# Performance work log

Measured on AMD Instinct MI355X. Metric: run time of the kernel, lower is better.

The kernel has to match this reference:

```python
import jax, jax.numpy as jnp
import numpy as np

NUM_HEADS = 16
HEAD_DIM = 128
WINDOW = 512
ROPE_BASE = 10000.0


def _rope_cos_sin(seq_len):
    inv_freq = 1.0 / (ROPE_BASE ** (jnp.arange(0, HEAD_DIM, 2, dtype=jnp.float32) / HEAD_DIM))
    freqs = jnp.arange(seq_len, dtype=jnp.float32)[:, None] * inv_freq[None, :]  # (s, d/2)
    return jnp.cos(freqs), jnp.sin(freqs)


def _apply_rotary(x, cos, sin):
    # x: (b, h, s, d); cos/sin: (s, d/2). Interleaved pairs as in the torch impl.
    x1, x2 = x[..., ::2], x[..., 1::2]
    c = cos[None, None]
    s = sin[None, None]
    r1 = x1 * c - x2 * s
    r2 = x1 * s + x2 * c
    return jnp.stack([r1, r2], axis=-1).reshape(x.shape)


def setup_inputs() -> dict:
    key = jax.random.key(0)
    ks = jax.random.split(key, 5)
    dim = NUM_HEADS * HEAD_DIM
    x = jax.random.normal(ks[0], (1, 4096, dim), dtype=jnp.float32)
    std = 0.02
    Wq = jax.random.normal(ks[1], (dim, dim), dtype=jnp.float32) * std
    Wk = jax.random.normal(ks[2], (dim, dim), dtype=jnp.float32) * std
    Wv = jax.random.normal(ks[3], (dim, dim), dtype=jnp.float32) * std
    Wo = jax.random.normal(ks[4], (dim, dim), dtype=jnp.float32) * std
    return {"x": x, "Wq": Wq, "Wk": Wk, "Wv": Wv, "Wo": Wo}


def reference(x, Wq, Wk, Wv, Wo):
    b, s, dim = x.shape
    scale = HEAD_DIM ** -0.5

    def split_heads(t):
        return t.reshape(b, s, NUM_HEADS, HEAD_DIM).transpose(0, 2, 1, 3)  # b h s d

    q = split_heads(x @ Wq.T)
    k = split_heads(x @ Wk.T)
    v = split_heads(x @ Wv.T)

    cos, sin = _rope_cos_sin(s)
    q = _apply_rotary(q, cos, sin)
    k = _apply_rotary(k, cos, sin)

    scores = jnp.einsum('bhqd,bhkd->bhqk', q, k) * scale  # (b, h, s, s)
    pos = jnp.arange(s)
    i, j = pos[:, None], pos[None, :]
    mask = (j <= i) & (i - j < WINDOW)  # sliding-window causal
    scores = jnp.where(mask[None, None], scores, -jnp.inf)
    attn = jax.nn.softmax(scores, axis=-1)

    out = jnp.einsum('bhqk,bhkd->bhqd', attn, v)
    out = out.transpose(0, 2, 1, 3).reshape(b, s, dim)
    return out @ Wo.T
```

## Files before the change

kernel.cpp:

```cpp
#include <hip/hip_runtime.h>
#include <hip/hip_bf16.h>
#include <math.h>

#define DIM 2048
#define NH 16
#define HD 128
#define WIN 512

typedef __hip_bfloat16 bf16;
using frag8 = __attribute__((ext_vector_type(8))) short;
using facc4 = __attribute__((ext_vector_type(4))) float;

__device__ inline float toF(const bf16 v) { return __bfloat162float(v); }
template <typename T> __device__ inline T fromF(float v);
template <> __device__ inline float fromF<float>(float v) { return v; }
template <> __device__ inline bf16 fromF<bf16>(float v) { return __float2bfloat16(v); }

__device__ inline unsigned bfb(float x) {
    unsigned u = __float_as_uint(x);
    u += 0x7fffu + ((u >> 16) & 1u);
    return u >> 16;
}

__device__ inline uint4 pack8(const float* p) {
    const float4 v0 = *(const float4*)p;
    const float4 v1 = *(const float4*)(p + 4);
    uint4 r;
    r.x = bfb(v0.x) | (bfb(v0.y) << 16);
    r.y = bfb(v0.z) | (bfb(v0.w) << 16);
    r.z = bfb(v1.x) | (bfb(v1.y) << 16);
    r.w = bfb(v1.z) | (bfb(v1.w) << 16);
    return r;
}

__global__ __launch_bounds__(256) void cvt_f32_bf16(const float* __restrict__ src,
                                                    bf16* __restrict__ dst, int n8) {
    const int i = blockIdx.x * 256 + threadIdx.x;
    if (i < n8) ((uint4*)dst)[i] = pack8(src + (size_t)i * 8);
}

#define W8LOG 19
__global__ __launch_bounds__(256) void cvt4_f32_bf16(const float* __restrict__ s0,
                                                     const float* __restrict__ s1,
                                                     const float* __restrict__ s2,
                                                     const float* __restrict__ s3,
                                                     bf16* __restrict__ dst) {
    const int i = blockIdx.x * 256 + threadIdx.x;
    const int seg = i >> W8LOG;
    const int off = i & ((1 << W8LOG) - 1);
    const float* s = (seg == 0) ? s0 : (seg == 1) ? s1 : (seg == 2) ? s2 : s3;
    ((uint4*)dst)[i] = pack8(s + (size_t)off * 8);
}

__device__ inline void gload_lds16(const bf16* g, short* l) {
    __builtin_amdgcn_global_load_lds(
        (const __attribute__((address_space(1))) unsigned int*)g,
        (__attribute__((address_space(3))) unsigned int*)l, 16, 0, 0);
}


#define WAIT_LGKM0()                                             \
    do {                                                         \
        asm volatile("s_waitcnt lgkmcnt(0)" ::: "memory");       \
        __builtin_amdgcn_sched_barrier(0);                       \
    } while (0)

#define READ_A(BUF, MI)                                                          \
    do {                                                                         \
        _Pragma("unroll") for (int ii = 0; ii < 4; ++ii)                         \
        _Pragma("unroll") for (int kk = 0; kk < 2; ++kk) {                       \
            const int row_ = wm * 128 + (MI) * 64 + ii * 16 + mr;                \
            const int slot_ = ((kk << 2) + q) ^ (row_ & 7);                      \
            a[ii][kk] = *(const frag8*)&lds[BUF][0][row_][slot_ << 3];           \
        }                                                                        \
    } while (0)

#define READ_B(BUF, NI)                                                          \
    do {                                                                         \
        _Pragma("unroll") for (int jj = 0; jj < 2; ++jj)                         \
        _Pragma("unroll") for (int kk = 0; kk < 2; ++kk) {                       \
            const int row_ = wn * 64 + (NI) * 32 + jj * 16 + mr;                 \
            const int slot_ = ((kk << 2) + q) ^ (row_ & 7);                      \
            b[NI][jj][kk] = *(const frag8*)&lds[BUF][1][row_][slot_ << 3];       \
        }                                                                        \
    } while (0)

#define MFMA_QUAD(MI, NI)                                                        \
    do {                                                                         \
        __builtin_amdgcn_s_setprio(1);                                           \
        _Pragma("unroll") for (int ii = 0; ii < 4; ++ii)                         \
        _Pragma("unroll") for (int jj = 0; jj < 2; ++jj)                         \
        _Pragma("unroll") for (int kk = 0; kk < 2; ++kk)                         \
            acc[(MI) * 4 + ii][(NI) * 2 + jj] =                                  \
                __builtin_amdgcn_mfma_f32_16x16x32_bf16(                         \
                    a[ii][kk], b[NI][jj][kk], acc[(MI) * 4 + ii][(NI) * 2 + jj], \
                    0, 0, 0);                                                    \
        __builtin_amdgcn_s_setprio(0);                                           \
    } while (0)

template <typename TC, bool SPLIT>
__global__ __launch_bounds__(512, 2) void gemm256_8ph(const bf16* __restrict__ A,
                                                      const bf16* __restrict__ B,
                                                      TC* __restrict__ C,
                                                      bf16* __restrict__ Qp,
                                                      bf16* __restrict__ Kp,
                                                      bf16* __restrict__ Vp,
                                                      int M, int N, int K) {
    __shared__ __align__(16) short lds[2][2][256][64];
    const int tid = threadIdx.x;
    const int lane = tid & 63;
    const int w = tid >> 6;

    const int gx = gridDim.x;
    const int nwg = gx * (int)gridDim.y;
    const int lin0 = (int)blockIdx.y * gx + (int)blockIdx.x;
    const int lin = ((nwg & 7) == 0) ? (lin0 & 7) * (nwg >> 3) + (lin0 >> 3) : lin0;
    const int n0 = (lin % gx) * 256;
    const int m0 = (lin / gx) * 256;

    const int wm = w >> 2, wn = w & 3;
    const int q = lane >> 4, mr = lane & 15;
    const int sl = lane & 7, rlo = lane >> 3;
    const int rbA = wm * 128 + wn * 16;
    const int rbB = (w >> 1) * 64 + (w & 1) * 16;

    const int nt = K >> 6;
    const int nIter = nt >> 1;

    facc4 acc[8][4];
#pragma unroll
    for (int i = 0; i < 8; ++i)
#pragma unroll
        for (int j = 0; j < 4; ++j)
#pragma unroll
            for (int r = 0; r < 4; ++r) acc[i][j][r] = 0.f;

    frag8 a[4][2], b[2][2][2];

    auto stage = [&](const bf16* __restrict__ G, int grb, int mat, int buf, int ub, int t) {
        const int kt = t < nt ? t : nt - 1;
        const int k0 = kt << 6;
#pragma unroll
        for (int u = 0; u < 2; ++u) {
            const int row0 = ub + u * 8;
            const int row = row0 + rlo;
            gload_lds16(G + (size_t)(grb + row) * K + k0 + ((sl ^ rlo) << 3),
                        (short*)&lds[buf][mat][row0][0]);
        }
    };

    stage(A, m0, 0, 0, rbA, 0);
    stage(A, m0, 0, 0, rbA + 64, 0);
    stage(B, n0, 1, 0, rbB, 0);
    stage(B, n0, 1, 0, rbB + 32, 0);
    stage(A, m0, 0, 1, rbA, 1);
    stage(B, n0, 1, 1, rbB, 1);
    stage(B, n0, 1, 1, rbB + 32, 1);
    asm volatile("s_waitcnt vmcnt(6)" ::: "memory");
    __builtin_amdgcn_s_barrier();

    for (int it = 0; it < nIter; ++it) {
        const int t2 = 2 * it + 2;
        READ_A(0, 0);
        READ_B(0, 0);
        stage(A, m0, 0, 1, rbA + 64, 2 * it + 1);
        __builtin_amdgcn_s_barrier();
        WAIT_LGKM0();
        MFMA_QUAD(0, 0);
        __builtin_amdgcn_s_barrier();
        READ_B(0, 1);
        stage(A, m0, 0, 0, rbA, t2);
        __builtin_amdgcn_s_barrier();
        WAIT_LGKM0();
        MFMA_QUAD(0, 1);
        __builtin_amdgcn_s_barrier();
        READ_A(0, 1);
        stage(B, n0, 1, 0, rbB, t2);
        __builtin_amdgcn_s_barrier();
        WAIT_LGKM0();
        MFMA_QUAD(1, 0);
        __builtin_amdgcn_s_barrier();
        stage(B, n0, 1, 0, rbB + 32, t2);
        __builtin_amdgcn_s_barrier();
        __builtin_amdgcn_sched_barrier(0);
        MFMA_QUAD(1, 1);
        asm volatile("s_waitcnt vmcnt(6)" ::: "memory");
        __builtin_amdgcn_s_barrier();
        READ_A(1, 0);
        READ_B(1, 0);
        stage(A, m0, 0, 0, rbA + 64, t2);
        __builtin_amdgcn_s_barrier();
        WAIT_LGKM0();
        MFMA_QUAD(0, 0);
        __builtin_amdgcn_s_barrier();
        READ_B(1, 1);
        stage(A, m0, 0, 1, rbA, t2 + 1);
        __builtin_amdgcn_s_barrier();
        WAIT_LGKM0();
        MFMA_QUAD(0, 1);
        __builtin_amdgcn_s_barrier();
        READ_A(1, 1);
        stage(B, n0, 1, 1, rbB, t2 + 1);
        __builtin_amdgcn_s_barrier();
        WAIT_LGKM0();
        MFMA_QUAD(1, 0);
        __builtin_amdgcn_s_barrier();
        stage(B, n0, 1, 1, rbB + 32, t2 + 1);
        __builtin_amdgcn_s_barrier();
        __builtin_amdgcn_sched_barrier(0);
        MFMA_QUAD(1, 1);
        asm volatile("s_waitcnt vmcnt(6)" ::: "memory");
        __builtin_amdgcn_s_barrier();
    }

    if (SPLIT) {
        if (n0 < 2 * DIM) {
            bf16* dst = (n0 < DIM) ? Qp : Kp;
            const int nb = n0 % DIM;
            const int row0 = m0 + wm * 128 + q * 4;
#pragma unroll
            for (int jn = 0; jn < 4; ++jn) {
                const int col = nb + wn * 64 + jn * 16 + mr;
                const int f = (col & 127) >> 1;
                const float inv = __expf(-0.14391157f * (float)f);
                const float sgn = (col & 1) ? 1.f : -1.f;
                float cb_, sb_, c1, s1, c16, s16;
                sincosf((float)row0 * inv, &sb_, &cb_);
                sincosf(inv, &s1, &c1);
                sincosf(16.f * inv, &s16, &c16);
#pragma unroll
                for (int im = 0; im < 8; ++im) {
                    float c = cb_, s = sb_;
#pragma unroll
                    for (int r = 0; r < 4; ++r) {
                        const float v = acc[im][jn][r];
                        const float p = __shfl_xor(v, 1, 64);
                        dst[(size_t)(row0 + im * 16 + r) * DIM + col] =
                            fromF<bf16>(v * c + sgn * p * s);
                        const float cn = c * c1 - s * s1;
                        const float sn = s * c1 + c * s1;
                        c = cn; s = sn;
                    }
                    const float cbn = cb_ * c16 - sb_ * s16;
                    const float sbn = sb_ * c16 + cb_ * s16;
                    cb_ = cbn; sb_ = sbn;
                }
            }
        } else {
            asm volatile("s_waitcnt vmcnt(0)" ::: "memory");
            __builtin_amdgcn_s_barrier();
            short* sc = (short*)lds;
            const int cb = n0 - 2 * DIM;
            const int colR = tid >> 2;
#pragma unroll
            for (int half = 0; half < 2; ++half) {
                if (half) __builtin_amdgcn_s_barrier();
                if ((wn >> 1) == half) {
#pragma unroll
                    for (int im = 0; im < 8; ++im) {
                        const int s = wm * 128 + im * 16 + q * 4;
#pragma unroll
                        for (int jn = 0; jn < 4; ++jn) {
                            const int cl = (wn & 1) * 64 + jn * 16 + mr;
                            uint2 pk;
                            pk.x = bfb(acc[im][jn][0]) | (bfb(acc[im][jn][1]) << 16);
                            pk.y = bfb(acc[im][jn][2]) | (bfb(acc[im][jn][3]) << 16);
                            *(uint2*)&sc[cl * 264 + s] = pk;
                        }
                    }
                }
                __builtin_amdgcn_s_barrier();
#pragma unroll
                for (int rr = 0; rr < 8; ++rr) {
                    const int s0 = (tid & 3) * 8 + rr * 32;
                    const uint4 v = *(const uint4*)&sc[colR * 264 + s0];
                    *(uint4*)(Vp + (size_t)(cb + half * 128 + colR) * M + m0 + s0) = v;
                }
            }
        }
    } else {
#pragma unroll
        for (int im = 0; im < 8; ++im)
#pragma unroll
            for (int jn = 0; jn < 4; ++jn) {
                const int col = n0 + wn * 64 + jn * 16 + mr;
#pragma unroll
                for (int r = 0; r < 4; ++r) {
                    const int row = m0 + wm * 128 + im * 16 + q * 4 + r;
                    C[(size_t)row * N + col] = fromF<TC>(acc[im][jn][r]);
                }
            }
    }
}

template <typename TC>
__global__ __launch_bounds__(256) void gemm_bt_async(const bf16* __restrict__ A,
                                                     const bf16* __restrict__ B,
                                                     TC* __restrict__ C,
                                                     int M, int N, int K) {
    __shared__ short As[128 * 32];
    __shared__ short Bs[128 * 32];
    const int tid = threadIdx.x;
    const int lane = tid & 63;
    const int w = tid >> 6;
    const int m0 = blockIdx.y * 128;
    const int n0 = blockIdx.x * 128;
    const int wm = (w >> 1) * 64;
    const int wn = (w & 1) * 64;
    const int q = lane >> 4;
    const int mr = lane & 15;

    facc4 acc[4][4];
#pragma unroll
    for (int i = 0; i < 4; ++i)
#pragma unroll
        for (int j = 0; j < 4; ++j)
#pragma unroll
            for (int r = 0; r < 4; ++r) acc[i][j][r] = 0.f;

    for (int k0 = 0; k0 < K; k0 += 32) {
        __syncthreads();
#pragma unroll
        for (int u = 0; u < 2; ++u) {
            const int c = w * 128 + u * 64 + lane;
            const int row = c >> 2, col = (c & 3) * 8;
            gload_lds16(A + (size_t)(m0 + row) * K + k0 + col, As + (w * 128 + u * 64) * 8);
            gload_lds16(B + (size_t)(n0 + row) * K + k0 + col, Bs + (w * 128 + u * 64) * 8);
        }
        __syncthreads();

        frag8 af[4], bfr[4];
#pragma unroll
        for (int i = 0; i < 4; ++i)
            af[i] = *(const frag8*)&As[(wm + 16 * i + mr) * 32 + q * 8];
#pragma unroll
        for (int j = 0; j < 4; ++j)
            bfr[j] = *(const frag8*)&Bs[(wn + 16 * j + mr) * 32 + q * 8];
#pragma unroll
        for (int i = 0; i < 4; ++i)
#pragma unroll
            for (int j = 0; j < 4; ++j)
                acc[i][j] = __builtin_amdgcn_mfma_f32_16x16x32_bf16(af[i], bfr[j], acc[i][j], 0, 0, 0);
    }

#pragma unroll
    for (int i = 0; i < 4; ++i)
#pragma unroll
        for (int j = 0; j < 4; ++j) {
            const int col = n0 + wn + 16 * j + mr;
#pragma unroll
            for (int r = 0; r < 4; ++r) {
                const int row = m0 + wm + 16 * i + q * 4 + r;
                C[(size_t)row * N + col] = fromF<TC>(acc[i][j][r]);
            }
        }
}

__global__ __launch_bounds__(256, 2) void flash_swa(const bf16* __restrict__ Q,
                                                    const bf16* __restrict__ K,
                                                    const bf16* __restrict__ Vt,
                                                    bf16* __restrict__ O, int S) {
    __shared__ __align__(16) char lds[74752];
    short* Ksl = (short*)lds;
    short* Vtl = (short*)(lds + 32768);
    short* Ps  = (short*)(lds + 65536);

    const int tid = threadIdx.x;
    const int lane = tid & 63;
    const int w = tid >> 6;
    const int q = lane >> 4;
    const int mr = lane & 15;
    const int bx = blockIdx.x;
    const int i0 = (((bx & 7) << 3) | (bx >> 3)) * 64;
    const int h = blockIdx.y;
    const float scale = 0.08838834764831845f;
    const int sw = mr & 7;

    frag8 qf[4];
    const bf16* qptr = Q + (size_t)(i0 + w * 16 + mr) * DIM + h * HD + q * 8;
#pragma unroll
    for (int kk = 0; kk < 4; ++kk) qf[kk] = *(const frag8*)(qptr + kk * 32);

    const bf16* vtg = Vt + (size_t)h * HD * S;

    int koff[4], voff[4];
#pragma unroll
    for (int u = 0; u < 4; ++u) {
        const int krow = w * 16 + 4 * u + (lane >> 4);
        const int kch = (lane & 15) ^ (krow & 7);
        koff[u] = krow * DIM + h * HD + kch * 8;
        const int vrow = w * 32 + 8 * u + (lane >> 3);
        const int vch = (lane & 7) ^ (vrow & 7);
        voff[u] = vrow * S + vch * 8;
    }

    auto issue = [&](int t, int buf) {
        int jb = i0 - WIN + t * 64;
        if (jb > S - 64) jb = S - 64;
        const bf16* kb = K + (size_t)jb * DIM;
        const bf16* vb = vtg + jb;
#pragma unroll
        for (int u = 0; u < 4; ++u)
            gload_lds16(kb + koff[u], Ksl + buf * 8192 + (w * 16 + 4 * u) * 128);
#pragma unroll
        for (int u = 0; u < 4; ++u)
            gload_lds16(vb + voff[u], Vtl + buf * 8192 + (w * 32 + 8 * u) * 64);
    };

    float mrow[4], lrow[4];
    facc4 oacc[8];
#pragma unroll
    for (int r = 0; r < 4; ++r) { mrow[r] = -1e30f; lrow[r] = 0.f; }
#pragma unroll
    for (int dt = 0; dt < 8; ++dt)
#pragma unroll
        for (int r = 0; r < 4; ++r) oacc[dt][r] = 0.f;

    const int t0 = (i0 >= WIN) ? 0 : (WIN - i0) / 64;
    issue(t0, 0);
    issue(t0 + 1, 1);
    int p = 0;

    for (int t = t0; t < 9; ++t) {
        const int jb = i0 - WIN + t * 64;
        asm volatile("s_waitcnt vmcnt(8)" ::: "memory");
        __builtin_amdgcn_s_barrier();
        __builtin_amdgcn_sched_barrier(0);

        facc4 sacc[4];
#pragma unroll
        for (int nt = 0; nt < 4; ++nt)
#pragma unroll
            for (int r = 0; r < 4; ++r) sacc[nt][r] = 0.f;
        __builtin_amdgcn_s_setprio(1);
#pragma unroll
        for (int nt = 0; nt < 4; ++nt) {
#pragma unroll
            for (int kk = 0; kk < 4; ++kk) {
                const frag8 kfr = *(const frag8*)&Ksl[p * 8192 + (nt * 16 + mr) * 128 +
                                                      (((kk * 4 + q) ^ sw) << 3)];
                sacc[nt] = __builtin_amdgcn_mfma_f32_16x16x32_bf16(qf[kk], kfr, sacc[nt], 0, 0, 0);
            }
        }
        __builtin_amdgcn_s_setprio(0);

        float sv[4][4];
        float rmax[4] = {-1e30f, -1e30f, -1e30f, -1e30f};
#pragma unroll
        for (int nt = 0; nt < 4; ++nt) {
            const int j = jb + nt * 16 + mr;
#pragma unroll
            for (int r = 0; r < 4; ++r) {
                const int i = i0 + w * 16 + q * 4 + r;
                const bool valid = (j <= i) && (i - j < WIN);
                sv[nt][r] = valid ? sacc[nt][r] * scale : -1e30f;
                rmax[r] = fmaxf(rmax[r], sv[nt][r]);
            }
        }
#pragma unroll
        for (int msk = 1; msk <= 8; msk <<= 1)
#pragma unroll
            for (int r = 0; r < 4; ++r)
                rmax[r] = fmaxf(rmax[r], __shfl_xor(rmax[r], msk, 64));

        float alpha[4], rsum[4];
#pragma unroll
        for (int r = 0; r < 4; ++r) {
            const float mn = fmaxf(mrow[r], rmax[r]);
            alpha[r] = __expf(mrow[r] - mn);
            mrow[r] = mn;
            rsum[r] = 0.f;
        }
#pragma unroll
        for (int nt = 0; nt < 4; ++nt)
#pragma unroll
            for (int r = 0; r < 4; ++r) {
                const float pv = (sv[nt][r] > -1e29f) ? __expf(sv[nt][r] - mrow[r]) : 0.f;
                rsum[r] += pv;
                Ps[(w * 16 + q * 4 + r) * 72 + nt * 16 + mr] = (short)bfb(pv);
            }
#pragma unroll
        for (int msk = 1; msk <= 8; msk <<= 1)
#pragma unroll
            for (int r = 0; r < 4; ++r)
                rsum[r] += __shfl_xor(rsum[r], msk, 64);
#pragma unroll
        for (int r = 0; r < 4; ++r) lrow[r] = lrow[r] * alpha[r] + rsum[r];
#pragma unroll
        for (int dt = 0; dt < 8; ++dt)
#pragma unroll
            for (int r = 0; r < 4; ++r) oacc[dt][r] *= alpha[r];

        __builtin_amdgcn_s_setprio(1);
#pragma unroll
        for (int ks = 0; ks < 2; ++ks) {
            const frag8 pf = *(const frag8*)&Ps[(w * 16 + mr) * 72 + ks * 32 + q * 8];
#pragma unroll
            for (int dt = 0; dt < 8; ++dt) {
                const frag8 vf = *(const frag8*)&Vtl[p * 8192 + (dt * 16 + mr) * 64 +
                                                     (((ks * 4 + q) ^ sw) << 3)];
                oacc[dt] = __builtin_amdgcn_mfma_f32_16x16x32_bf16(pf, vf, oacc[dt], 0, 0, 0);
            }
        }
        __builtin_amdgcn_s_setprio(0);

        __builtin_amdgcn_s_barrier();
        __builtin_amdgcn_sched_barrier(0);
        issue(t + 2, p);
        p ^= 1;
    }
    asm volatile("s_waitcnt vmcnt(0)" ::: "memory");

    float inv[4];
#pragma unroll
    for (int r = 0; r < 4; ++r) inv[r] = 1.0f / lrow[r];
#pragma unroll
    for (int dt = 0; dt < 8; ++dt)
#pragma unroll
        for (int r = 0; r < 4; ++r) {
            const int row = i0 + w * 16 + q * 4 + r;
            O[(size_t)row * DIM + h * HD + dt * 16 + mr] = fromF<bf16>(oacc[dt][r] * inv[r]);
        }
}

extern "C" void kernel_launch(void* const* d_in, const int* in_sizes, int n_in,
                              void* d_out, int out_size, void* d_ws, size_t ws_size,
                              hipStream_t stream) {
    const float* x  = (const float*)d_in[0];
    const float* Wq = (const float*)d_in[1];
    const float* Wk = (const float*)d_in[2];
    const float* Wv = (const float*)d_in[3];
    const float* Wo = (const float*)d_in[4];
    float* out = (float*)d_out;

    const int S = in_sizes[0] / DIM;
    const size_t elems = (size_t)S * DIM;
    const size_t wsz = (size_t)DIM * DIM;

    bf16* Q    = (bf16*)d_ws;
    bf16* K    = Q + elems;
    bf16* V    = K + elems;
    bf16* Aat  = V + elems;
    bf16* xb   = Aat + elems;
    bf16* Wcat = xb + elems;
    bf16* Wob  = Wcat + 3 * wsz;

    cvt_f32_bf16<<<(int)(elems / 8 / 256), 256, 0, stream>>>(x, xb, (int)(elems / 8));
    cvt4_f32_bf16<<<(int)(4 * wsz / 8 / 256), 256, 0, stream>>>(Wq, Wk, Wv, Wo, Wcat);

    gemm256_8ph<bf16, true><<<dim3(3 * DIM / 256, S / 256), 512, 0, stream>>>(
        xb, Wcat, (bf16*)nullptr, Q, K, V, S, 3 * DIM, DIM);

    flash_swa<<<dim3(S / 64, NH), 256, 0, stream>>>(Q, K, V, Aat, S);

    gemm_bt_async<float><<<dim3(DIM / 128, S / 128), 256, 0, stream>>>(
        Aat, Wob, out, S, DIM, DIM);
}
```

Before: 375.5 us.

## Enlarge flash SWA query tile to 256 rows with 8 waves, two row groups each

Each flash-attention block now handles 256 query rows with 8 waves, and each wave processes two 16-row groups. This lets each K/V tile loaded into LDS be reused across four times as many queries, and the V fragment is shared across both groups in the PV MFMA loop. The block-to-(head, query tile) mapping is also reworked so neighbouring blocks share K/V from adjacent heads. In exchange, the key-tile loop runs 12 iterations instead of 9 to cover the wider window, so more partially masked tiles are computed. Register pressure and LDS use per block also rise, which may reduce occupancy.

```diff
diff --git a/kernel.cpp b/kernel.cpp
--- a/kernel.cpp
+++ b/kernel.cpp
@@ -356,11 +356,11 @@
         }
 }
 
-__global__ __launch_bounds__(256, 2) void flash_swa(const bf16* __restrict__ Q,
+__global__ __launch_bounds__(512, 2) void flash_swa(const bf16* __restrict__ Q,
                                                     const bf16* __restrict__ K,
                                                     const bf16* __restrict__ Vt,
                                                     bf16* __restrict__ O, int S) {
-    __shared__ __align__(16) char lds[74752];
+    __shared__ __align__(16) char lds[102400];
     short* Ksl = (short*)lds;
     short* Vtl = (short*)(lds + 32768);
     short* Ps  = (short*)(lds + 65536);
@@ -370,28 +370,29 @@
     const int w = tid >> 6;
     const int q = lane >> 4;
     const int mr = lane & 15;
-    const int bx = blockIdx.x;
-    const int i0 = (((bx & 7) << 3) | (bx >> 3)) * 64;
-    const int h = blockIdx.y;
+    const int lin = (int)blockIdx.y * (int)gridDim.x + (int)blockIdx.x;
+    const int h = (lin & 7) * 2 + ((lin >> 3) & 1);
+    const int i0 = (lin >> 4) * 256;
     const float scale = 0.08838834764831845f;
     const int sw = mr & 7;
 
-    frag8 qf[4];
-    const bf16* qptr = Q + (size_t)(i0 + w * 16 + mr) * DIM + h * HD + q * 8;
-#pragma unroll
-    for (int kk = 0; kk < 4; ++kk) qf[kk] = *(const frag8*)(qptr + kk * 32);
+    frag8 qf[2][4];
+#pragma unroll
+    for (int g = 0; g < 2; ++g) {
+        const bf16* qptr = Q + (size_t)(i0 + w * 32 + g * 16 + mr) * DIM + h * HD + q * 8;
+#pragma unroll
+        for (int kk = 0; kk < 4; ++kk) qf[g][kk] = *(const frag8*)(qptr + kk * 32);
+    }
 
     const bf16* vtg = Vt + (size_t)h * HD * S;
 
-    int koff[4], voff[4];
-#pragma unroll
-    for (int u = 0; u < 4; ++u) {
-        const int krow = w * 16 + 4 * u + (lane >> 4);
-        const int kch = (lane & 15) ^ (krow & 7);
-        koff[u] = krow * DIM + h * HD + kch * 8;
-        const int vrow = w * 32 + 8 * u + (lane >> 3);
-        const int vch = (lane & 7) ^ (vrow & 7);
-        voff[u] = vrow * S + vch * 8;
+    int koff[2], voff[2];
+#pragma unroll
+    for (int u = 0; u < 2; ++u) {
+        const int krow = w * 8 + u * 4 + (lane >> 4);
+        koff[u] = krow * DIM + h * HD + (((lane & 15) ^ (krow & 7)) << 3);
+        const int vrow = w * 16 + u * 8 + (lane >> 3);
+        voff[u] = vrow * S + (((lane & 7) ^ (vrow & 7)) << 3);
     }
 
     auto issue = [&](int t, int buf) {
@@ -400,106 +401,114 @@
         const bf16* kb = K + (size_t)jb * DIM;
         const bf16* vb = vtg + jb;
 #pragma unroll
-        for (int u = 0; u < 4; ++u)
-            gload_lds16(kb + koff[u], Ksl + buf * 8192 + (w * 16 + 4 * u) * 128);
-#pragma unroll
-        for (int u = 0; u < 4; ++u)
-            gload_lds16(vb + voff[u], Vtl + buf * 8192 + (w * 32 + 8 * u) * 64);
+        for (int u = 0; u < 2; ++u)
+            gload_lds16(kb + koff[u], Ksl + buf * 8192 + w * 1024 + u * 512);
+#pragma unroll
+        for (int u = 0; u < 2; ++u)
+            gload_lds16(vb + voff[u], Vtl + buf * 8192 + w * 1024 + u * 512);
     };
 
-    float mrow[4], lrow[4];
-    facc4 oacc[8];
-#pragma unroll
-    for (int r = 0; r < 4; ++r) { mrow[r] = -1e30f; lrow[r] = 0.f; }
-#pragma unroll
-    for (int dt = 0; dt < 8; ++dt)
-#pragma unroll
-        for (int r = 0; r < 4; ++r) oacc[dt][r] = 0.f;
+    float mrow[2][4], lrow[2][4];
+    facc4 oacc[2][8];
+#pragma unroll
+    for (int g = 0; g < 2; ++g) {
+#pragma unroll
+        for (int r = 0; r < 4; ++r) { mrow[g][r] = -1e30f; lrow[g][r] = 0.f; }
+#pragma unroll
+        for (int dt = 0; dt < 8; ++dt)
+#pragma unroll
+            for (int r = 0; r < 4; ++r) oacc[g][dt][r] = 0.f;
+    }
 
     const int t0 = (i0 >= WIN) ? 0 : (WIN - i0) / 64;
     issue(t0, 0);
     issue(t0 + 1, 1);
     int p = 0;
 
-    for (int t = t0; t < 9; ++t) {
+    for (int t = t0; t < 12; ++t) {
         const int jb = i0 - WIN + t * 64;
-        asm volatile("s_waitcnt vmcnt(8)" ::: "memory");
+        asm volatile("s_waitcnt vmcnt(4)" ::: "memory");
         __builtin_amdgcn_s_barrier();
         __builtin_amdgcn_sched_barrier(0);
 
-        facc4 sacc[4];
-#pragma unroll
-        for (int nt = 0; nt < 4; ++nt)
-#pragma unroll
-            for (int r = 0; r < 4; ++r) sacc[nt][r] = 0.f;
+#pragma unroll
+        for (int g = 0; g < 2; ++g) {
+            facc4 sacc[4];
+#pragma unroll
+            for (int nt = 0; nt < 4; ++nt)
+#pragma unroll
+                for (int r = 0; r < 4; ++r) sacc[nt][r] = 0.f;
+            __builtin_amdgcn_s_setprio(1);
+#pragma unroll
+            for (int nt = 0; nt < 4; ++nt) {
+#pragma unroll
+                for (int kk = 0; kk < 4; ++kk) {
+                    const frag8 kfr = *(const frag8*)&Ksl[p * 8192 + (nt * 16 + mr) * 128 +
+                                                          (((kk * 4 + q) ^ sw) << 3)];
+                    sacc[nt] = __builtin_amdgcn_mfma_f32_16x16x32_bf16(qf[g][kk], kfr, sacc[nt], 0, 0, 0);
+                }
+            }
+            __builtin_amdgcn_s_setprio(0);
+
+            float sv[4][4];
+            float rmax[4] = {-1e30f, -1e30f, -1e30f, -1e30f};
+#pragma unroll
+            for (int nt = 0; nt < 4; ++nt) {
+                const int j = jb + nt * 16 + mr;
+#pragma unroll
+                for (int r = 0; r < 4; ++r) {
+                    const int i = i0 + w * 32 + g * 16 + q * 4 + r;
+                    const bool valid = (j <= i) && (i - j < WIN);
+                    sv[nt][r] = valid ? sacc[nt][r] * scale : -1e30f;
+                    rmax[r] = fmaxf(rmax[r], sv[nt][r]);
+                }
+            }
+#pragma unroll
+            for (int msk = 1; msk <= 8; msk <<= 1)
+#pragma unroll
+                for (int r = 0; r < 4; ++r)
+                    rmax[r] = fmaxf(rmax[r], __shfl_xor(rmax[r], msk, 64));
+
+            float alpha[4], rsum[4];
+#pragma unroll
+            for (int r = 0; r < 4; ++r) {
+                const float mn = fmaxf(mrow[g][r], rmax[r]);
+                alpha[r] = __expf(mrow[g][r] - mn);
+                mrow[g][r] = mn;
+                rsum[r] = 0.f;
+            }
+#pragma unroll
+            for (int nt = 0; nt < 4; ++nt)
+#pragma unroll
+                for (int r = 0; r < 4; ++r) {
+                    const float pv = (sv[nt][r] > -1e29f) ? __expf(sv[nt][r] - mrow[g][r]) : 0.f;
+                    rsum[r] += pv;
+                    Ps[(w * 32 + g * 16 + q * 4 + r) * 72 + nt * 16 + mr] = (short)bfb(pv);
+                }
+#pragma unroll
+            for (int msk = 1; msk <= 8; msk <<= 1)
+#pragma unroll
+                for (int r = 0; r < 4; ++r)
+                    rsum[r] += __shfl_xor(rsum[r], msk, 64);
+#pragma unroll
+            for (int r = 0; r < 4; ++r) lrow[g][r] = lrow[g][r] * alpha[r] + rsum[r];
+#pragma unroll
+            for (int dt = 0; dt < 8; ++dt)
+#pragma unroll
+                for (int r = 0; r < 4; ++r) oacc[g][dt][r] *= alpha[r];
+        }
+
         __builtin_amdgcn_s_setprio(1);
 #pragma unroll
-        for (int nt = 0; nt < 4; ++nt) {
-#pragma unroll
-            for (int kk = 0; kk < 4; ++kk) {
-                const frag8 kfr = *(const frag8*)&Ksl[p * 8192 + (nt * 16 + mr) * 128 +
-                                                      (((kk * 4 + q) ^ sw) << 3)];
-                sacc[nt] = __builtin_amdgcn_mfma_f32_16x16x32_bf16(qf[kk], kfr, sacc[nt], 0, 0, 0);
-            }
-        }
-        __builtin_amdgcn_s_setprio(0);
-
-        float sv[4][4];
-        float rmax[4] = {-1e30f, -1e30f, -1e30f, -1e30f};
-#pragma unroll
-        for (int nt = 0; nt < 4; ++nt) {
-            const int j = jb + nt * 16 + mr;
-#pragma unroll
-            for (int r = 0; r < 4; ++r) {
-                const int i = i0 + w * 16 + q * 4 + r;
-                const bool valid = (j <= i) && (i - j < WIN);
-                sv[nt][r] = valid ? sacc[nt][r] * scale : -1e30f;
-                rmax[r] = fmaxf(rmax[r], sv[nt][r]);
-            }
-        }
-#pragma unroll
-        for (int msk = 1; msk <= 8; msk <<= 1)
-#pragma unroll
-            for (int r = 0; r < 4; ++r)
-                rmax[r] = fmaxf(rmax[r], __shfl_xor(rmax[r], msk, 64));
-
-        float alpha[4], rsum[4];
-#pragma unroll
-        for (int r = 0; r < 4; ++r) {
-            const float mn = fmaxf(mrow[r], rmax[r]);
-            alpha[r] = __expf(mrow[r] - mn);
-            mrow[r] = mn;
-            rsum[r] = 0.f;
-        }
-#pragma unroll
-        for (int nt = 0; nt < 4; ++nt)
-#pragma unroll
-            for (int r = 0; r < 4; ++r) {
-                const float pv = (sv[nt][r] > -1e29f) ? __expf(sv[nt][r] - mrow[r]) : 0.f;
-                rsum[r] += pv;
-                Ps[(w * 16 + q * 4 + r) * 72 + nt * 16 + mr] = (short)bfb(pv);
-            }
-#pragma unroll
-        for (int msk = 1; msk <= 8; msk <<= 1)
-#pragma unroll
-            for (int r = 0; r < 4; ++r)
-                rsum[r] += __shfl_xor(rsum[r], msk, 64);
-#pragma unroll
-        for (int r = 0; r < 4; ++r) lrow[r] = lrow[r] * alpha[r] + rsum[r];
-#pragma unroll
-        for (int dt = 0; dt < 8; ++dt)
-#pragma unroll
-            for (int r = 0; r < 4; ++r) oacc[dt][r] *= alpha[r];
-
-        __builtin_amdgcn_s_setprio(1);
-#pragma unroll
         for (int ks = 0; ks < 2; ++ks) {
-            const frag8 pf = *(const frag8*)&Ps[(w * 16 + mr) * 72 + ks * 32 + q * 8];
+            const frag8 pf0 = *(const frag8*)&Ps[(w * 32 + mr) * 72 + ks * 32 + q * 8];
+            const frag8 pf1 = *(const frag8*)&Ps[(w * 32 + 16 + mr) * 72 + ks * 32 + q * 8];
 #pragma unroll
             for (int dt = 0; dt < 8; ++dt) {
                 const frag8 vf = *(const frag8*)&Vtl[p * 8192 + (dt * 16 + mr) * 64 +
                                                      (((ks * 4 + q) ^ sw) << 3)];
-                oacc[dt] = __builtin_amdgcn_mfma_f32_16x16x32_bf16(pf, vf, oacc[dt], 0, 0, 0);
+                oacc[0][dt] = __builtin_amdgcn_mfma_f32_16x16x32_bf16(pf0, vf, oacc[0][dt], 0, 0, 0);
+                oacc[1][dt] = __builtin_amdgcn_mfma_f32_16x16x32_bf16(pf1, vf, oacc[1][dt], 0, 0, 0);
             }
         }
         __builtin_amdgcn_s_setprio(0);
@@ -511,16 +520,19 @@
     }
     asm volatile("s_waitcnt vmcnt(0)" ::: "memory");
 
-    float inv[4];
-#pragma unroll
-    for (int r = 0; r < 4; ++r) inv[r] = 1.0f / lrow[r];
-#pragma unroll
-    for (int dt = 0; dt < 8; ++dt)
-#pragma unroll
-        for (int r = 0; r < 4; ++r) {
-            const int row = i0 + w * 16 + q * 4 + r;
-            O[(size_t)row * DIM + h * HD + dt * 16 + mr] = fromF<bf16>(oacc[dt][r] * inv[r]);
-        }
+#pragma unroll
+    for (int g = 0; g < 2; ++g) {
+        float inv[4];
+#pragma unroll
+        for (int r = 0; r < 4; ++r) inv[r] = 1.0f / lrow[g][r];
+#pragma unroll
+        for (int dt = 0; dt < 8; ++dt)
+#pragma unroll
+            for (int r = 0; r < 4; ++r) {
+                const int row = i0 + w * 32 + g * 16 + q * 4 + r;
+                O[(size_t)row * DIM + h * HD + dt * 16 + mr] = fromF<bf16>(oacc[g][dt][r] * inv[r]);
+            }
+    }
 }
 
 extern "C" void kernel_launch(void* const* d_in, const int* in_sizes, int n_in,
@@ -551,7 +563,7 @@
     gemm256_8ph<bf16, true><<<dim3(3 * DIM / 256, S / 256), 512, 0, stream>>>(
         xb, Wcat, (bf16*)nullptr, Q, K, V, S, 3 * DIM, DIM);
 
-    flash_swa<<<dim3(S / 64, NH), 256, 0, stream>>>(Q, K, V, Aat, S);
+    flash_swa<<<dim3(S / 256, NH), 512, 0, stream>>>(Q, K, V, Aat, S);
 
     gemm_bt_async<float><<<dim3(DIM / 128, S / 128), 256, 0, stream>>>(
         Aat, Wob, out, S, DIM, DIM);
```

New measurement: 383.2 us. 1.02x slower.
